# Kernel tuning notes

Hardware: AMD Instinct MI355X
Metric: run time of the kernel (lower is better)

The kernel has to match this reference:

```python
import jax, jax.numpy as jnp
import numpy as np

N_NODES = 100000
N_EDGES = 600000
D = 128


def setup_inputs() -> dict:
    key = jax.random.key(0)
    k1, k2, k3, k4, k5, k6 = jax.random.split(key, 6)
    src_x = jax.random.normal(k1, (N_NODES, D), dtype=jnp.float32)
    dst_x = jax.random.normal(k2, (N_NODES, D), dtype=jnp.float32)
    edge_index = jax.random.randint(k3, (2, N_EDGES), 0, N_NODES, dtype=jnp.int32)
    edge_weight = jax.random.uniform(k4, (N_EDGES, 1), dtype=jnp.float32)
    # xavier-uniform square weights: bound = sqrt(6/(fan_in+fan_out))
    bound = float(np.sqrt(6.0 / (D + D)))
    W_intra = jax.random.uniform(k5, (D, D), dtype=jnp.float32, minval=-bound, maxval=bound)
    W_inter = jax.random.uniform(k6, (D, D), dtype=jnp.float32, minval=-bound, maxval=bound)
    return {"src_x": src_x, "dst_x": dst_x, "edge_index": edge_index,
            "edge_weight": edge_weight, "W_intra": W_intra, "W_inter": W_inter}


def reference(src_x, dst_x, edge_index, edge_weight, W_intra, W_inter):
    # Inference mode: node_dropout / message_dropout are identity.
    src_idx, dst_idx = edge_index[0], edge_index[1]
    # self-to-self messages: transform source nodes once, then gather per edge
    intra_src = src_x @ W_intra.T                      # [N, D]
    s2s_msgs = intra_src[src_idx]                      # [E, D]
    # interaction messages: elementwise src*dst per edge, then transform
    i2s_msgs = (src_x[src_idx] * dst_x[dst_idx]) @ W_inter.T  # [E, D]
    src_msgs = edge_weight * (s2s_msgs + i2s_msgs)     # [E, D]
    self_msg = dst_x @ W_intra.T                       # [N, D]
    # scatter-add messages into destination nodes
    src_msg = jax.ops.segment_sum(src_msgs, dst_idx, num_segments=dst_x.shape[0])
    return jax.nn.leaky_relu(self_msg + src_msg, negative_slope=0.01)
```

## Files before the change

kernel.cpp:

```cpp
#include <hip/hip_runtime.h>
#include <hip/hip_bf16.h>

#define N_NODES 100000
#define N_EDGES 600000
#define D 128
#define ROWS_PB 32
#define NBLK_F (N_NODES / ROWS_PB)
#define CAPN 32
#define GSTR 132

typedef __attribute__((ext_vector_type(8))) short short8;
typedef __attribute__((ext_vector_type(8))) unsigned short ushort8;
typedef __attribute__((ext_vector_type(4))) float f32x4;
typedef __attribute__((ext_vector_type(2))) int i32x2;
typedef __attribute__((ext_vector_type(2))) float f32x2;

union V8 { short8 s8; ushort8 u8; };

__device__ __forceinline__ unsigned short f2bf(float f) {
    unsigned u = __float_as_uint(f);
    u += 0x7FFF + ((u >> 16) & 1);
    return (unsigned short)(u >> 16);
}

__global__ void wfrag_kernel(const float* __restrict__ Wi,
                             const float* __restrict__ We,
                             unsigned short* __restrict__ Wfi,
                             unsigned short* __restrict__ Wfe,
                             unsigned* __restrict__ cur) {
    int id = blockIdx.x * blockDim.x + threadIdx.x;
    for (int j = id; j < N_NODES; j += 16384) cur[j] = 0u;
    if (id >= 4096) return;
    int mat = id >> 11;
    int idx = id & 2047;
    int lane = idx & 63;
    int ks = (idx >> 6) & 3;
    int nt = idx >> 8;
    int n = lane & 15, quad = lane >> 4;
    int row = nt * 16 + n;
    int k0 = ks * 32 + quad * 8;
    const float* W = mat ? We : Wi;
    unsigned short* Wf = mat ? Wfe : Wfi;
    #pragma unroll
    for (int j = 0; j < 8; ++j)
        Wf[idx * 8 + j] = f2bf(W[row * D + k0 + j]);
}

__global__ void scatter_kernel(const i32x2* __restrict__ src2,
                               const i32x2* __restrict__ dst2,
                               const f32x2* __restrict__ ew2,
                               unsigned* __restrict__ cur,
                               i32x2* __restrict__ bkt) {
    int i = blockIdx.x * blockDim.x + threadIdx.x;
    if (i < N_EDGES / 2) {
        i32x2 s = __builtin_nontemporal_load(&src2[i]);
        i32x2 d = __builtin_nontemporal_load(&dst2[i]);
        f32x2 wv = __builtin_nontemporal_load(&ew2[i]);
        unsigned p0 = atomicAdd(&cur[d[0]], 1u);
        unsigned p1 = atomicAdd(&cur[d[1]], 1u);
        if (p0 < CAPN) {
            i32x2 m = {s[0], __float_as_int(wv[0])};
            __builtin_nontemporal_store(m, &bkt[(size_t)d[0] * CAPN + p0]);
        }
        if (p1 < CAPN) {
            i32x2 m = {s[1], __float_as_int(wv[1])};
            __builtin_nontemporal_store(m, &bkt[(size_t)d[1] * CAPN + p1]);
        }
    }
}

__global__ __launch_bounds__(256, 4) void fused_kernel(
    const float* __restrict__ src_x,
    const float* __restrict__ dst_x,
    const i32x2* __restrict__ bkt,
    const unsigned* __restrict__ cur,
    const unsigned short* __restrict__ Wfi,
    const unsigned short* __restrict__ Wfe,
    float* __restrict__ out) {
    __shared__ float g[ROWS_PB * GSTR];

    int t = threadIdx.x, lane = t & 63, w = t >> 6;
    int quad = lane >> 4, nl = lane & 15;
    int qid = t >> 4;
    int lbase = (lane >> 4) << 4;

    int b = blockIdx.x, d0 = b * ROWS_PB;

    #pragma unroll
    for (int half = 0; half < 2; ++half) {
        int r = 2 * qid + half;
        int node = d0 + r;
        int cn = (int)cur[node];
        if (cn > CAPN) cn = CAPN;
        const i32x2* bp = bkt + (size_t)node * CAPN;
        i32x2 mA = __builtin_nontemporal_load(&bp[nl]);
        i32x2 mB = __builtin_nontemporal_load(&bp[nl + 16]);
        float4 a = {0.f, 0.f, 0.f, 0.f}, c = {0.f, 0.f, 0.f, 0.f};
        if (cn > 0) {
            int s0 = __shfl(mA[0], lbase);
            float w0 = __int_as_float(__shfl(mA[1], lbase));
            int i1 = (cn > 1) ? 1 : 0;
            int s1 = __shfl(mA[0], lbase | i1);
            float w1 = __int_as_float(__shfl(mA[1], lbase | i1));
            const float* p0 = src_x + (size_t)s0 * D + nl * 8;
            float4 A0 = *(const float4*)p0, B0 = *(const float4*)(p0 + 4);
            const float* p1 = src_x + (size_t)s1 * D + nl * 8;
            float4 A1 = *(const float4*)p1, B1 = *(const float4*)(p1 + 4);
            for (int e = 0; e < cn; ++e) {
                int k = e + 2; if (k > cn - 1) k = cn - 1;
                int srcl = lbase | (k & 15);
                int sk = __shfl(k < 16 ? mA[0] : mB[0], srcl);
                float wk = __int_as_float(__shfl(k < 16 ? mA[1] : mB[1], srcl));
                const float* pk = src_x + (size_t)sk * D + nl * 8;
                float4 A2 = *(const float4*)pk, B2 = *(const float4*)(pk + 4);
                a.x += w0 * A0.x; a.y += w0 * A0.y;
                a.z += w0 * A0.z; a.w += w0 * A0.w;
                c.x += w0 * B0.x; c.y += w0 * B0.y;
                c.z += w0 * B0.z; c.w += w0 * B0.w;
                A0 = A1; B0 = B1; w0 = w1;
                A1 = A2; B1 = B2; w1 = wk;
            }
        }
        float* gp = &g[r * GSTR + nl * 8];
        *(float4*)gp = a;
        *(float4*)(gp + 4) = c;
    }
    __syncthreads();

    const short8* Wiv = (const short8*)Wfi;
    const short8* Wev = (const short8*)Wfe;
    short8 Bi[2][4], Be[2][4];
    #pragma unroll
    for (int ntl = 0; ntl < 2; ++ntl)
        #pragma unroll
        for (int ks = 0; ks < 4; ++ks) {
            Bi[ntl][ks] = Wiv[((2 * w + ntl) * 4 + ks) * 64 + lane];
            Be[ntl][ks] = Wev[((2 * w + ntl) * 4 + ks) * 64 + lane];
        }

    #pragma unroll
    for (int tl = 0; tl < 2; ++tl) {
        int r = tl * 16 + nl;
        const float* xr = dst_x + (size_t)(d0 + r) * D + quad * 8;
        const float* gr = &g[r * GSTR + quad * 8];
        f32x4 acc[2];
        acc[0] = (f32x4){0.f, 0.f, 0.f, 0.f};
        acc[1] = (f32x4){0.f, 0.f, 0.f, 0.f};
        #pragma unroll
        for (int ks = 0; ks < 4; ++ks) {
            float4 f0 = *(const float4*)(xr + ks * 32);
            float4 f1 = *(const float4*)(xr + ks * 32 + 4);
            float4 g0 = *(const float4*)(gr + ks * 32);
            float4 g1 = *(const float4*)(gr + ks * 32 + 4);
            V8 a1v, a2v;
            a1v.u8[0] = f2bf(f0.x + g0.x); a2v.u8[0] = f2bf(f0.x * g0.x);
            a1v.u8[1] = f2bf(f0.y + g0.y); a2v.u8[1] = f2bf(f0.y * g0.y);
            a1v.u8[2] = f2bf(f0.z + g0.z); a2v.u8[2] = f2bf(f0.z * g0.z);
            a1v.u8[3] = f2bf(f0.w + g0.w); a2v.u8[3] = f2bf(f0.w * g0.w);
            a1v.u8[4] = f2bf(f1.x + g1.x); a2v.u8[4] = f2bf(f1.x * g1.x);
            a1v.u8[5] = f2bf(f1.y + g1.y); a2v.u8[5] = f2bf(f1.y * g1.y);
            a1v.u8[6] = f2bf(f1.z + g1.z); a2v.u8[6] = f2bf(f1.z * g1.z);
            a1v.u8[7] = f2bf(f1.w + g1.w); a2v.u8[7] = f2bf(f1.w * g1.w);
            acc[0] = __builtin_amdgcn_mfma_f32_16x16x32_bf16(a1v.s8, Bi[0][ks], acc[0], 0, 0, 0);
            acc[1] = __builtin_amdgcn_mfma_f32_16x16x32_bf16(a1v.s8, Bi[1][ks], acc[1], 0, 0, 0);
            acc[0] = __builtin_amdgcn_mfma_f32_16x16x32_bf16(a2v.s8, Be[0][ks], acc[0], 0, 0, 0);
            acc[1] = __builtin_amdgcn_mfma_f32_16x16x32_bf16(a2v.s8, Be[1][ks], acc[1], 0, 0, 0);
        }
        #pragma unroll
        for (int ntl = 0; ntl < 2; ++ntl)
            #pragma unroll
            for (int rr = 0; rr < 4; ++rr) {
                float v = acc[ntl][rr];
                v = v > 0.f ? v : 0.01f * v;
                out[(size_t)(d0 + tl * 16 + quad * 4 + rr) * D
                    + (2 * w + ntl) * 16 + nl] = v;
            }
    }
}

extern "C" void kernel_launch(void* const* d_in, const int* in_sizes, int n_in,
                              void* d_out, int out_size, void* d_ws, size_t ws_size,
                              hipStream_t stream) {
    const float* src_x = (const float*)d_in[0];
    const float* dst_x = (const float*)d_in[1];
    const int*   eidx  = (const int*)d_in[2];
    const float* ew    = (const float*)d_in[3];
    const float* Wi    = (const float*)d_in[4];
    const float* We    = (const float*)d_in[5];
    float* out = (float*)d_out;

    char* wsb = (char*)d_ws;
    unsigned short* Wfi = (unsigned short*)(wsb);
    unsigned short* Wfe = (unsigned short*)(wsb + 32768);
    unsigned* cur = (unsigned*)(wsb + 65536);
    i32x2* bkt = (i32x2*)(wsb + 65536 + 400000);

    const int* src_idx = eidx;
    const int* dst_idx = eidx + N_EDGES;

    wfrag_kernel<<<64, 256, 0, stream>>>(Wi, We, Wfi, Wfe, cur);

    scatter_kernel<<<(N_EDGES / 2 + 255) / 256, 256, 0, stream>>>(
        (const i32x2*)src_idx, (const i32x2*)dst_idx, (const f32x2*)ew,
        cur, bkt);

    fused_kernel<<<NBLK_F, 256, 0, stream>>>(
        src_x, dst_x, bkt, cur, Wfi, Wfe, out);
}
```

Measured before the change: 246.2 us.

## Fuse three launches into one cooperative persistent kernel with grid syncs

```diff
diff --git a/kernel.cpp b/kernel.cpp
--- a/kernel.cpp
+++ b/kernel.cpp
@@ -1,13 +1,18 @@
 #include <hip/hip_runtime.h>
 #include <hip/hip_bf16.h>
+#include <hip/hip_cooperative_groups.h>
+
+namespace cg = cooperative_groups;
 
 #define N_NODES 100000
 #define N_EDGES 600000
 #define D 128
 #define ROWS_PB 32
-#define NBLK_F (N_NODES / ROWS_PB)
+#define NTILE (N_NODES / ROWS_PB)
 #define CAPN 32
 #define GSTR 132
+#define GRID_B 1024
+#define NTHR (GRID_B * 256)
 
 typedef __attribute__((ext_vector_type(8))) short short8;
 typedef __attribute__((ext_vector_type(8))) unsigned short ushort8;
@@ -23,14 +28,10 @@
     return (unsigned short)(u >> 16);
 }
 
-__global__ void wfrag_kernel(const float* __restrict__ Wi,
-                             const float* __restrict__ We,
-                             unsigned short* __restrict__ Wfi,
-                             unsigned short* __restrict__ Wfe,
-                             unsigned* __restrict__ cur) {
-    int id = blockIdx.x * blockDim.x + threadIdx.x;
-    for (int j = id; j < N_NODES; j += 16384) cur[j] = 0u;
-    if (id >= 4096) return;
+__device__ __forceinline__ void wfrag_body(int id, const float* Wi,
+                                           const float* We,
+                                           unsigned short* Wfi,
+                                           unsigned short* Wfe) {
     int mat = id >> 11;
     int idx = id & 2047;
     int lane = idx & 63;
@@ -46,45 +47,17 @@
         Wf[idx * 8 + j] = f2bf(W[row * D + k0 + j]);
 }
 
-__global__ void scatter_kernel(const i32x2* __restrict__ src2,
-                               const i32x2* __restrict__ dst2,
-                               const f32x2* __restrict__ ew2,
-                               unsigned* __restrict__ cur,
-                               i32x2* __restrict__ bkt) {
-    int i = blockIdx.x * blockDim.x + threadIdx.x;
-    if (i < N_EDGES / 2) {
-        i32x2 s = __builtin_nontemporal_load(&src2[i]);
-        i32x2 d = __builtin_nontemporal_load(&dst2[i]);
-        f32x2 wv = __builtin_nontemporal_load(&ew2[i]);
-        unsigned p0 = atomicAdd(&cur[d[0]], 1u);
-        unsigned p1 = atomicAdd(&cur[d[1]], 1u);
-        if (p0 < CAPN) {
-            i32x2 m = {s[0], __float_as_int(wv[0])};
-            __builtin_nontemporal_store(m, &bkt[(size_t)d[0] * CAPN + p0]);
-        }
-        if (p1 < CAPN) {
-            i32x2 m = {s[1], __float_as_int(wv[1])};
-            __builtin_nontemporal_store(m, &bkt[(size_t)d[1] * CAPN + p1]);
-        }
-    }
-}
-
-__global__ __launch_bounds__(256, 4) void fused_kernel(
-    const float* __restrict__ src_x,
-    const float* __restrict__ dst_x,
-    const i32x2* __restrict__ bkt,
-    const unsigned* __restrict__ cur,
+__device__ __forceinline__ void fused_tile(
+    int d0, int t, float* g,
+    const float* __restrict__ src_x, const float* __restrict__ dst_x,
+    const i32x2* __restrict__ bkt, const unsigned* __restrict__ cur,
     const unsigned short* __restrict__ Wfi,
     const unsigned short* __restrict__ Wfe,
     float* __restrict__ out) {
-    __shared__ float g[ROWS_PB * GSTR];
-
-    int t = threadIdx.x, lane = t & 63, w = t >> 6;
+    int lane = t & 63, w = t >> 6;
     int quad = lane >> 4, nl = lane & 15;
     int qid = t >> 4;
     int lbase = (lane >> 4) << 4;
-
-    int b = blockIdx.x, d0 = b * ROWS_PB;
 
     #pragma unroll
     for (int half = 0; half < 2; ++half) {
@@ -178,6 +151,94 @@
     }
 }
 
+__global__ __launch_bounds__(256, 4) void mono_kernel(
+    const float* __restrict__ src_x,
+    const float* __restrict__ dst_x,
+    const int* __restrict__ src_idx,
+    const int* __restrict__ dst_idx,
+    const float* __restrict__ ew,
+    const float* __restrict__ Wi,
+    const float* __restrict__ We,
+    unsigned short* __restrict__ Wfi,
+    unsigned short* __restrict__ Wfe,
+    unsigned* __restrict__ cur,
+    i32x2* __restrict__ bkt,
+    float* __restrict__ out) {
+    __shared__ float g[ROWS_PB * GSTR];
+
+    cg::grid_group grid = cg::this_grid();
+    int t = threadIdx.x;
+    int gid = blockIdx.x * 256 + t;
+
+    if (gid < N_NODES) cur[gid] = 0u;
+    if (gid < 4096) wfrag_body(gid, Wi, We, Wfi, Wfe);
+    grid.sync();
+
+    for (int e = gid; e < N_EDGES; e += NTHR) {
+        int s = src_idx[e];
+        int d = dst_idx[e];
+        float wv = ew[e];
+        unsigned pos = atomicAdd(&cur[d], 1u);
+        if (pos < CAPN) {
+            i32x2 m = {s, __float_as_int(wv)};
+            bkt[(size_t)d * CAPN + pos] = m;
+        }
+    }
+    grid.sync();
+
+    for (int tile = blockIdx.x; tile < NTILE; tile += GRID_B) {
+        fused_tile(tile * ROWS_PB, t, g, src_x, dst_x, bkt, cur, Wfi, Wfe, out);
+        __syncthreads();
+    }
+}
+
+__global__ void wfrag_kernel(const float* __restrict__ Wi,
+                             const float* __restrict__ We,
+                             unsigned short* __restrict__ Wfi,
+                             unsigned short* __restrict__ Wfe,
+                             unsigned* __restrict__ cur) {
+    int id = blockIdx.x * blockDim.x + threadIdx.x;
+    for (int j = id; j < N_NODES; j += 16384) cur[j] = 0u;
+    if (id >= 4096) return;
+    wfrag_body(id, Wi, We, Wfi, Wfe);
+}
+
+__global__ void scatter_kernel(const i32x2* __restrict__ src2,
+                               const i32x2* __restrict__ dst2,
+                               const f32x2* __restrict__ ew2,
+                               unsigned* __restrict__ cur,
+                               i32x2* __restrict__ bkt) {
+    int i = blockIdx.x * blockDim.x + threadIdx.x;
+    if (i < N_EDGES / 2) {
+        i32x2 s = __builtin_nontemporal_load(&src2[i]);
+        i32x2 d = __builtin_nontemporal_load(&dst2[i]);
+        f32x2 wv = __builtin_nontemporal_load(&ew2[i]);
+        unsigned p0 = atomicAdd(&cur[d[0]], 1u);
+        unsigned p1 = atomicAdd(&cur[d[1]], 1u);
+        if (p0 < CAPN) {
+            i32x2 m = {s[0], __float_as_int(wv[0])};
+            __builtin_nontemporal_store(m, &bkt[(size_t)d[0] * CAPN + p0]);
+        }
+        if (p1 < CAPN) {
+            i32x2 m = {s[1], __float_as_int(wv[1])};
+            __builtin_nontemporal_store(m, &bkt[(size_t)d[1] * CAPN + p1]);
+        }
+    }
+}
+
+__global__ __launch_bounds__(256, 4) void fused_kernel(
+    const float* __restrict__ src_x,
+    const float* __restrict__ dst_x,
+    const i32x2* __restrict__ bkt,
+    const unsigned* __restrict__ cur,
+    const unsigned short* __restrict__ Wfi,
+    const unsigned short* __restrict__ Wfe,
+    float* __restrict__ out) {
+    __shared__ float g[ROWS_PB * GSTR];
+    fused_tile(blockIdx.x * ROWS_PB, threadIdx.x, g,
+               src_x, dst_x, bkt, cur, Wfi, Wfe, out);
+}
+
 extern "C" void kernel_launch(void* const* d_in, const int* in_sizes, int n_in,
                               void* d_out, int out_size, void* d_ws, size_t ws_size,
                               hipStream_t stream) {
@@ -198,12 +259,19 @@
     const int* src_idx = eidx;
     const int* dst_idx = eidx + N_EDGES;
 
-    wfrag_kernel<<<64, 256, 0, stream>>>(Wi, We, Wfi, Wfe, cur);
-
-    scatter_kernel<<<(N_EDGES / 2 + 255) / 256, 256, 0, stream>>>(
-        (const i32x2*)src_idx, (const i32x2*)dst_idx, (const f32x2*)ew,
-        cur, bkt);
-
-    fused_kernel<<<NBLK_F, 256, 0, stream>>>(
-        src_x, dst_x, bkt, cur, Wfi, Wfe, out);
-}
+    void* args[] = {
+        (void*)&src_x, (void*)&dst_x, (void*)&src_idx, (void*)&dst_idx,
+        (void*)&ew, (void*)&Wi, (void*)&We,
+        (void*)&Wfi, (void*)&Wfe, (void*)&cur, (void*)&bkt, (void*)&out
+    };
+    hipError_t err = hipLaunchCooperativeKernel(
+        (const void*)mono_kernel, dim3(GRID_B), dim3(256), args, 0, stream);
+    if (err != hipSuccess) {
+        wfrag_kernel<<<64, 256, 0, stream>>>(Wi, We, Wfi, Wfe, cur);
+        scatter_kernel<<<(N_EDGES / 2 + 255) / 256, 256, 0, stream>>>(
+            (const i32x2*)src_idx, (const i32x2*)dst_idx, (const f32x2*)ew,
+            cur, bkt);
+        fused_kernel<<<NTILE, 256, 0, stream>>>(
+            src_x, dst_x, bkt, cur, Wfi, Wfe, out);
+    }
+}
```

New measurement: 443.7 us. 1.8x slower.
